# Kernel optimization log

Measured on AMD Instinct MI355X. Metric: run time of the kernel, lower is better.

The kernel has to match this reference:

```python
import jax, jax.numpy as jnp
import numpy as np
import math

B, S, H = 4, 2048, 1024
EMBED_DIM = 1024


def setup_inputs() -> dict:
    key = jax.random.key(0)
    ks = jax.random.split(key, 7)
    scale = 1.0 / math.sqrt(H)
    return {
        "xs": jax.random.normal(ks[0], (B, S, H), dtype=jnp.float32),
        "WQ_w": jax.random.normal(ks[1], (EMBED_DIM, H), dtype=jnp.float32) * scale,
        "WQ_b": jax.random.normal(ks[2], (EMBED_DIM,), dtype=jnp.float32) * scale,
        "WK_w": jax.random.normal(ks[3], (EMBED_DIM, H), dtype=jnp.float32) * scale,
        "WK_b": jax.random.normal(ks[4], (EMBED_DIM,), dtype=jnp.float32) * scale,
        "WV_w": jax.random.normal(ks[5], (EMBED_DIM, H), dtype=jnp.float32) * scale,
        "WV_b": jax.random.normal(ks[6], (EMBED_DIM,), dtype=jnp.float32) * scale,
    }


def reference(xs, WQ_w, WQ_b, WK_w, WK_b, WV_w, WV_b):
    # Linear projections (torch nn.Linear: x @ W.T + b)
    q = jnp.einsum('bsh,eh->bse', xs, WQ_w) + WQ_b  # [B,S,E]
    k = jnp.einsum('bsh,eh->bse', xs, WK_w) + WK_b
    v = jnp.einsum('bsh,eh->bse', xs, WV_w) + WV_b
    seq_len = xs.shape[1]
    inv_sqrt_e = 1.0 / math.sqrt(EMBED_DIM)
    qk = jnp.einsum('bqe,bke->bqk', q, k) * inv_sqrt_e  # [B,S,S]
    # causal mask: positions k > q get -inf (triu, diagonal=1)
    causal = jnp.tril(jnp.ones((seq_len, seq_len), dtype=bool))
    qk = jnp.where(causal[None, :, :], qk, -jnp.inf)
    attn = jax.nn.softmax(qk, axis=2)
    y = jnp.einsum('bqk,bke->bqe', attn, v)  # [B,S,E]
    return y
```

## Files before the change

kernel.cpp:

```cpp
#include <hip/hip_runtime.h>
#include <cstdint>
#include <cstddef>

typedef _Float16 f16;
typedef __attribute__((ext_vector_type(4))) _Float16 f16x4;
typedef __attribute__((ext_vector_type(8))) _Float16 f16x8;
typedef __attribute__((ext_vector_type(4))) float f32x4;

static constexpr int BB = 4;
static constexpr int SS = 2048;
static constexpr int EE = 1024;

static constexpr int BM = 128, BN = 128, BK = 32;

__device__ __forceinline__ void gload_lds16(const f16* g, f16* l) {
  __builtin_amdgcn_global_load_lds(
      (const __attribute__((address_space(1))) void*)g,
      (__attribute__((address_space(3))) void*)l, 16, 0, 0);
}

struct Frag {
  int lane, wave, wy, wx, l16, quad;
  __device__ Frag() {
    const int tid = threadIdx.x;
    lane = tid & 63; wave = tid >> 6;
    wy = wave >> 1; wx = wave & 1;
    l16 = lane & 15; quad = lane >> 4;
  }
};

__device__ __forceinline__ void gemm_core(
    const f16* __restrict__ A, const f16* __restrict__ Bt,
    int lda, int ldb, int kTiles,
    f16* __restrict__ Ash, f16* __restrict__ Bsh,
    f32x4 acc[4][4], const Frag& fr)
{
  const int ca0 = fr.wave * 128 + fr.lane;
  const int ca1 = ca0 + 64;
  const int ra0 = ca0 >> 2, ka0 = (ca0 & 3) << 3;
  const int ra1 = ca1 >> 2, ka1 = (ca1 & 3) << 3;

  const f16* gA0 = A + (size_t)ra0 * lda + ka0;
  const f16* gA1 = A + (size_t)ra1 * lda + ka1;
  const f16* gB0 = Bt + (size_t)ra0 * ldb + ka0;
  const f16* gB1 = Bt + (size_t)ra1 * ldb + ka1;
  f16* lA0 = Ash + ca0 * 8;
  f16* lA1 = Ash + ca1 * 8;
  f16* lB0 = Bsh + ca0 * 8;
  f16* lB1 = Bsh + ca1 * 8;

  for (int kt = 0; kt < kTiles; ++kt) {
    const int ko = kt * BK;
    gload_lds16(gA0 + ko, lA0);
    gload_lds16(gA1 + ko, lA1);
    gload_lds16(gB0 + ko, lB0);
    gload_lds16(gB1 + ko, lB1);
    __syncthreads();
    f16x8 af[4], bf[4];
#pragma unroll
    for (int mi = 0; mi < 4; ++mi)
      af[mi] = *(const f16x8*)(Ash + (fr.wy * 64 + mi * 16 + fr.l16) * BK + fr.quad * 8);
#pragma unroll
    for (int ni = 0; ni < 4; ++ni)
      bf[ni] = *(const f16x8*)(Bsh + (fr.wx * 64 + ni * 16 + fr.l16) * BK + fr.quad * 8);
#pragma unroll
    for (int mi = 0; mi < 4; ++mi)
#pragma unroll
      for (int ni = 0; ni < 4; ++ni)
        acc[mi][ni] = __builtin_amdgcn_mfma_f32_16x16x32_f16(af[mi], bf[ni], acc[mi][ni], 0, 0, 0);
    __syncthreads();
  }
}

__global__ __launch_bounds__(256) void cast_kernel(
    const float* __restrict__ in, f16* __restrict__ out, int n4)
{
  const int i = blockIdx.x * 256 + threadIdx.x;
  if (i < n4) {
    const float4 f = ((const float4*)in)[i];
    f16x4 h;
    h.x = (f16)f.x; h.y = (f16)f.y; h.z = (f16)f.z; h.w = (f16)f.w;
    ((f16x4*)out)[i] = h;
  }
}

__global__ __launch_bounds__(256) void cast_w_kernel(
    const float* __restrict__ w0, const float* __restrict__ w1, const float* __restrict__ w2,
    f16* __restrict__ o0, f16* __restrict__ o1, f16* __restrict__ o2, int n4)
{
  const int z = blockIdx.y;
  const float* in = (z == 0) ? w0 : (z == 1) ? w1 : w2;
  f16* out = (z == 0) ? o0 : (z == 1) ? o1 : o2;
  const int i = blockIdx.x * 256 + threadIdx.x;
  if (i < n4) {
    const float4 f = ((const float4*)in)[i];
    f16x4 h;
    h.x = (f16)f.x; h.y = (f16)f.y; h.z = (f16)f.z; h.w = (f16)f.w;
    ((f16x4*)out)[i] = h;
  }
}

__global__ __launch_bounds__(256, 4) void qkv_kernel(
    const f16* __restrict__ X,
    const f16* __restrict__ W0, const f16* __restrict__ W1, const f16* __restrict__ W2,
    const float* __restrict__ b0, const float* __restrict__ b1, const float* __restrict__ b2,
    f16* __restrict__ O0, f16* __restrict__ O1, f16* __restrict__ O2)
{
  __shared__ __align__(16) f16 Ash[BM * BK];
  __shared__ __align__(16) f16 Bsh[BN * BK];
  const int z = blockIdx.z;
  const f16* W = (z == 0) ? W0 : (z == 1) ? W1 : W2;
  const float* bias = (z == 0) ? b0 : (z == 1) ? b1 : b2;
  f16* out = (z == 0) ? O0 : (z == 1) ? O1 : O2;
  const int row0 = blockIdx.x * BM, col0 = blockIdx.y * BN;
  Frag fr;
  f32x4 acc[4][4] = {};
  gemm_core(X + (size_t)row0 * EE, W + (size_t)col0 * EE, EE, EE, EE / BK, Ash, Bsh, acc, fr);
#pragma unroll
  for (int ni = 0; ni < 4; ++ni) {
    const int c = col0 + fr.wx * 64 + ni * 16 + fr.l16;
    const float bv = bias[c];
#pragma unroll
    for (int mi = 0; mi < 4; ++mi) {
      const int r = row0 + fr.wy * 64 + mi * 16 + fr.quad * 4;
#pragma unroll
      for (int i = 0; i < 4; ++i)
        out[(size_t)(r + i) * EE + c] = (f16)(acc[mi][ni][i] + bv);
    }
  }
}

__global__ __launch_bounds__(256) void transpose_kernel(
    const f16* __restrict__ V, f16* __restrict__ Vt)
{
  __shared__ __align__(16) f16 t[64][68];
  const int b = blockIdx.z;
  const int s0 = blockIdx.x * 64, e0 = blockIdx.y * 64;
  const int tid = threadIdx.x;
  const int r = tid >> 4;
  const int c4 = (tid & 15) << 2;
  const f16* src = V + (size_t)b * SS * EE;
  f16* dst = Vt + (size_t)b * EE * SS;
#pragma unroll
  for (int i = 0; i < 4; ++i) {
    const int row = i * 16 + r;
    const f16x4 v = *(const f16x4*)(src + (size_t)(s0 + row) * EE + e0 + c4);
    *(f16x4*)&t[row][c4] = v;
  }
  __syncthreads();
#pragma unroll
  for (int i = 0; i < 4; ++i) {
    const int row = i * 16 + r;
    f16x4 v;
    v.x = t[c4 + 0][row]; v.y = t[c4 + 1][row];
    v.z = t[c4 + 2][row]; v.w = t[c4 + 3][row];
    *(f16x4*)(dst + (size_t)(e0 + row) * SS + s0 + c4) = v;
  }
}

__global__ __launch_bounds__(256, 4) void scores_kernel(
    const f16* __restrict__ Q, const f16* __restrict__ Kh, f16* __restrict__ Sc)
{
  __shared__ __align__(16) f16 Ash[BM * BK];
  __shared__ __align__(16) f16 Bsh[BN * BK];
  const int t = blockIdx.x, b = blockIdx.z;
  int qt = 0;
  while ((qt + 1) * (qt + 2) / 2 <= t) ++qt;
  const int kt = t - qt * (qt + 1) / 2;
  const f16* A  = Q  + (size_t)b * SS * EE + (size_t)qt * BM * EE;
  const f16* Bp = Kh + (size_t)b * SS * EE + (size_t)kt * BN * EE;
  f16* out = Sc + (size_t)b * SS * SS;
  Frag fr;
  f32x4 acc[4][4] = {};
  gemm_core(A, Bp, EE, EE, EE / BK, Ash, Bsh, acc, fr);
  const float scale = 0.03125f;
#pragma unroll
  for (int ni = 0; ni < 4; ++ni) {
    const int c = kt * BN + fr.wx * 64 + ni * 16 + fr.l16;
#pragma unroll
    for (int mi = 0; mi < 4; ++mi) {
      const int r = qt * BM + fr.wy * 64 + mi * 16 + fr.quad * 4;
#pragma unroll
      for (int i = 0; i < 4; ++i)
        out[(size_t)(r + i) * SS + c] = (f16)(acc[mi][ni][i] * scale);
    }
  }
}

__global__ __launch_bounds__(256) void softmax_kernel(f16* __restrict__ Sc)
{
  const int q = blockIdx.x, b = blockIdx.y;
  f16* row = Sc + (size_t)b * SS * SS + (size_t)q * SS;
  const int n = q + 1;
  const int kend = ((q >> 7) + 1) << 7;
  const int tid = threadIdx.x;
  const int i0 = tid * 8;

  float v[8];
  if (i0 + 8 <= n) {
    const f16x8 h = *(const f16x8*)(row + i0);
#pragma unroll
    for (int j = 0; j < 8; ++j) v[j] = (float)h[j];
  } else {
#pragma unroll
    for (int j = 0; j < 8; ++j) {
      const int idx = i0 + j;
      v[j] = (idx < n) ? (float)row[idx] : -1e30f;
    }
  }

  float m = v[0];
#pragma unroll
  for (int j = 1; j < 8; ++j) m = fmaxf(m, v[j]);
  __shared__ float red[4];
#pragma unroll
  for (int off = 32; off > 0; off >>= 1) m = fmaxf(m, __shfl_down(m, off));
  if ((tid & 63) == 0) red[tid >> 6] = m;
  __syncthreads();
  m = fmaxf(fmaxf(red[0], red[1]), fmaxf(red[2], red[3]));

  float sum = 0.f;
#pragma unroll
  for (int j = 0; j < 8; ++j) {
    v[j] = (i0 + j < n) ? __expf(v[j] - m) : 0.f;
    sum += v[j];
  }
#pragma unroll
  for (int off = 32; off > 0; off >>= 1) sum += __shfl_down(sum, off);
  __syncthreads();
  if ((tid & 63) == 0) red[tid >> 6] = sum;
  __syncthreads();
  sum = red[0] + red[1] + red[2] + red[3];
  const float inv = 1.f / sum;

  if (i0 < kend) {
    f16x8 h;
#pragma unroll
    for (int j = 0; j < 8; ++j) h[j] = (f16)(v[j] * inv);
    *(f16x8*)(row + i0) = h;
  }
}

__global__ __launch_bounds__(256, 4) void pv_kernel(
    const f16* __restrict__ P, const f16* __restrict__ Vt, float* __restrict__ Y)
{
  __shared__ __align__(16) f16 Ash[BM * BK];
  __shared__ __align__(16) f16 Bsh[BN * BK];
  const int qt = (gridDim.x - 1) - blockIdx.x, et = blockIdx.y, b = blockIdx.z;
  const f16* A  = P  + (size_t)b * SS * SS + (size_t)qt * BM * SS;
  const f16* Bp = Vt + (size_t)b * EE * SS + (size_t)et * BN * SS;
  float* out = Y + (size_t)b * SS * EE;
  Frag fr;
  f32x4 acc[4][4] = {};
  gemm_core(A, Bp, SS, SS, (qt + 1) * (BM / BK), Ash, Bsh, acc, fr);
#pragma unroll
  for (int ni = 0; ni < 4; ++ni) {
    const int c = et * BN + fr.wx * 64 + ni * 16 + fr.l16;
#pragma unroll
    for (int mi = 0; mi < 4; ++mi) {
      const int r = qt * BM + fr.wy * 64 + mi * 16 + fr.quad * 4;
#pragma unroll
      for (int i = 0; i < 4; ++i)
        out[(size_t)(r + i) * EE + c] = acc[mi][ni][i];
    }
  }
}

extern "C" void kernel_launch(void* const* d_in, const int* in_sizes, int n_in,
                              void* d_out, int out_size, void* d_ws, size_t ws_size,
                              hipStream_t stream)
{
  const float* xs  = (const float*)d_in[0];
  const float* WQw = (const float*)d_in[1];
  const float* WQb = (const float*)d_in[2];
  const float* WKw = (const float*)d_in[3];
  const float* WKb = (const float*)d_in[4];
  const float* WVw = (const float*)d_in[5];
  const float* WVb = (const float*)d_in[6];

  const size_t ME = (size_t)BB * SS * EE;
  const size_t WE = (size_t)EE * EE;

  f16* Xh = (f16*)d_ws;
  f16* Wq = Xh + ME;
  f16* Wk = Wq + WE;
  f16* Wv = Wk + WE;
  f16* Qh = Wv + WE;
  f16* Kh = Qh + ME;
  f16* Vh = Kh + ME;
  f16* Vt = Vh + ME;
  f16* Sc = Vt + ME;

  cast_kernel<<<dim3((unsigned)(ME / 4 / 256)), 256, 0, stream>>>(xs, Xh, (int)(ME / 4));
  cast_w_kernel<<<dim3((unsigned)(WE / 4 / 256), 3), 256, 0, stream>>>(
      WQw, WKw, WVw, Wq, Wk, Wv, (int)(WE / 4));

  qkv_kernel<<<dim3((BB * SS) / BM, EE / BN, 3), 256, 0, stream>>>(
      Xh, Wq, Wk, Wv, WQb, WKb, WVb, Qh, Kh, Vh);
  transpose_kernel<<<dim3(SS / 64, EE / 64, BB), 256, 0, stream>>>(Vh, Vt);
  const int nTri = (SS / BM) * (SS / BM + 1) / 2;
  scores_kernel<<<dim3(nTri, 1, BB), 256, 0, stream>>>(Qh, Kh, Sc);
  softmax_kernel<<<dim3(SS, BB), 256, 0, stream>>>(Sc);
  pv_kernel<<<dim3(SS / BM, EE / BN, BB), 256, 0, stream>>>(Sc, Vt, (float*)d_out);
}
```

Baseline: 267.8 us.

## Switch GEMMs to 256x128 tiles with 32x32x16 MFMA and swizzled LDS

Enlarges the shared GEMM core's block tile to 256x128 and moves from 16x16x32 to 32x32x16 MFMA, so each wave computes a 128x64 sub-tile from fewer LDS fragment loads. It adds an XOR swizzle on the K-chunk index of the LDS layout to cut bank conflicts. The causal score tiling, softmax padding and PV loop bounds are adjusted to the 256-row query tiles. The cost is more accumulator registers (occupancy hint drops from 4 to 2 blocks), coarser causal granularity that computes more masked-out work, and fewer blocks in the grids.

```diff
diff --git a/kernel.cpp b/kernel.cpp
--- a/kernel.cpp
+++ b/kernel.cpp
@@ -5,13 +5,13 @@
 typedef _Float16 f16;
 typedef __attribute__((ext_vector_type(4))) _Float16 f16x4;
 typedef __attribute__((ext_vector_type(8))) _Float16 f16x8;
-typedef __attribute__((ext_vector_type(4))) float f32x4;
+typedef __attribute__((ext_vector_type(16))) float f32x16;
 
 static constexpr int BB = 4;
 static constexpr int SS = 2048;
 static constexpr int EE = 1024;
 
-static constexpr int BM = 128, BN = 128, BK = 32;
+static constexpr int BM = 256, BN = 128, BK = 32;
 
 __device__ __forceinline__ void gload_lds16(const f16* g, f16* l) {
   __builtin_amdgcn_global_load_lds(
@@ -20,54 +20,69 @@
 }
 
 struct Frag {
-  int lane, wave, wy, wx, l16, quad;
+  int lane, wave, wy, wx, l32, lh;
   __device__ Frag() {
     const int tid = threadIdx.x;
     lane = tid & 63; wave = tid >> 6;
     wy = wave >> 1; wx = wave & 1;
-    l16 = lane & 15; quad = lane >> 4;
+    l32 = lane & 31; lh = lane >> 5;
   }
 };
 
 __device__ __forceinline__ void gemm_core(
     const f16* __restrict__ A, const f16* __restrict__ Bt,
-    int lda, int ldb, int kTiles,
+    int lda, int ldb, int kIters,
     f16* __restrict__ Ash, f16* __restrict__ Bsh,
-    f32x4 acc[4][4], const Frag& fr)
-{
-  const int ca0 = fr.wave * 128 + fr.lane;
-  const int ca1 = ca0 + 64;
-  const int ra0 = ca0 >> 2, ka0 = (ca0 & 3) << 3;
-  const int ra1 = ca1 >> 2, ka1 = (ca1 & 3) << 3;
-
-  const f16* gA0 = A + (size_t)ra0 * lda + ka0;
-  const f16* gA1 = A + (size_t)ra1 * lda + ka1;
-  const f16* gB0 = Bt + (size_t)ra0 * ldb + ka0;
-  const f16* gB1 = Bt + (size_t)ra1 * ldb + ka1;
-  f16* lA0 = Ash + ca0 * 8;
-  f16* lA1 = Ash + ca1 * 8;
-  f16* lB0 = Bsh + ca0 * 8;
-  f16* lB1 = Bsh + ca1 * 8;
-
-  for (int kt = 0; kt < kTiles; ++kt) {
+    f32x16 acc[4][2], const Frag& fr)
+{
+  const f16* gA[4]; f16* lA[4];
+#pragma unroll
+  for (int i = 0; i < 4; ++i) {
+    const int c = fr.wave * 256 + i * 64 + fr.lane;
+    const int row = c >> 2;
+    const int kc = (c & 3) ^ (row & 3);
+    gA[i] = A + (size_t)row * lda + kc * 8;
+    lA[i] = Ash + c * 8;
+  }
+  const f16* gB[2]; f16* lB[2];
+#pragma unroll
+  for (int i = 0; i < 2; ++i) {
+    const int c = fr.wave * 128 + i * 64 + fr.lane;
+    const int row = c >> 2;
+    const int kc = (c & 3) ^ (row & 3);
+    gB[i] = Bt + (size_t)row * ldb + kc * 8;
+    lB[i] = Bsh + c * 8;
+  }
+  int aoff[2], boff[2];
+#pragma unroll
+  for (int ks = 0; ks < 2; ++ks) {
+    const int perm = ((ks * 2 + fr.lh) ^ (fr.l32 & 3)) * 8;
+    aoff[ks] = (fr.wy * 128 + fr.l32) * 32 + perm;
+    boff[ks] = (fr.wx * 64 + fr.l32) * 32 + perm;
+  }
+
+  for (int kt = 0; kt < kIters; ++kt) {
     const int ko = kt * BK;
-    gload_lds16(gA0 + ko, lA0);
-    gload_lds16(gA1 + ko, lA1);
-    gload_lds16(gB0 + ko, lB0);
-    gload_lds16(gB1 + ko, lB1);
+#pragma unroll
+    for (int i = 0; i < 4; ++i) gload_lds16(gA[i] + ko, lA[i]);
+#pragma unroll
+    for (int i = 0; i < 2; ++i) gload_lds16(gB[i] + ko, lB[i]);
     __syncthreads();
-    f16x8 af[4], bf[4];
-#pragma unroll
-    for (int mi = 0; mi < 4; ++mi)
-      af[mi] = *(const f16x8*)(Ash + (fr.wy * 64 + mi * 16 + fr.l16) * BK + fr.quad * 8);
-#pragma unroll
-    for (int ni = 0; ni < 4; ++ni)
-      bf[ni] = *(const f16x8*)(Bsh + (fr.wx * 64 + ni * 16 + fr.l16) * BK + fr.quad * 8);
-#pragma unroll
-    for (int mi = 0; mi < 4; ++mi)
-#pragma unroll
-      for (int ni = 0; ni < 4; ++ni)
-        acc[mi][ni] = __builtin_amdgcn_mfma_f32_16x16x32_f16(af[mi], bf[ni], acc[mi][ni], 0, 0, 0);
+#pragma unroll
+    for (int ks = 0; ks < 2; ++ks) {
+      f16x8 af[4], bf[2];
+#pragma unroll
+      for (int mi = 0; mi < 4; ++mi)
+        af[mi] = *(const f16x8*)(Ash + aoff[ks] + mi * 32 * 32);
+#pragma unroll
+      for (int ni = 0; ni < 2; ++ni)
+        bf[ni] = *(const f16x8*)(Bsh + boff[ks] + ni * 32 * 32);
+#pragma unroll
+      for (int mi = 0; mi < 4; ++mi)
+#pragma unroll
+        for (int ni = 0; ni < 2; ++ni)
+          acc[mi][ni] = __builtin_amdgcn_mfma_f32_32x32x16_f16(af[mi], bf[ni], acc[mi][ni], 0, 0, 0);
+    }
     __syncthreads();
   }
 }
@@ -100,7 +115,7 @@
   }
 }
 
-__global__ __launch_bounds__(256, 4) void qkv_kernel(
+__global__ __launch_bounds__(256, 2) void qkv_kernel(
     const f16* __restrict__ X,
     const f16* __restrict__ W0, const f16* __restrict__ W1, const f16* __restrict__ W2,
     const float* __restrict__ b0, const float* __restrict__ b1, const float* __restrict__ b2,
@@ -114,18 +129,20 @@
   f16* out = (z == 0) ? O0 : (z == 1) ? O1 : O2;
   const int row0 = blockIdx.x * BM, col0 = blockIdx.y * BN;
   Frag fr;
-  f32x4 acc[4][4] = {};
+  f32x16 acc[4][2] = {};
   gemm_core(X + (size_t)row0 * EE, W + (size_t)col0 * EE, EE, EE, EE / BK, Ash, Bsh, acc, fr);
 #pragma unroll
-  for (int ni = 0; ni < 4; ++ni) {
-    const int c = col0 + fr.wx * 64 + ni * 16 + fr.l16;
+  for (int ni = 0; ni < 2; ++ni) {
+    const int c = col0 + fr.wx * 64 + ni * 32 + fr.l32;
     const float bv = bias[c];
 #pragma unroll
     for (int mi = 0; mi < 4; ++mi) {
-      const int r = row0 + fr.wy * 64 + mi * 16 + fr.quad * 4;
-#pragma unroll
-      for (int i = 0; i < 4; ++i)
-        out[(size_t)(r + i) * EE + c] = (f16)(acc[mi][ni][i] + bv);
+      const int rbase = row0 + fr.wy * 128 + mi * 32 + fr.lh * 4;
+#pragma unroll
+      for (int i = 0; i < 16; ++i) {
+        const int r = rbase + (i & 3) + 8 * (i >> 2);
+        out[(size_t)r * EE + c] = (f16)(acc[mi][ni][i] + bv);
+      }
     }
   }
 }
@@ -158,31 +175,33 @@
   }
 }
 
-__global__ __launch_bounds__(256, 4) void scores_kernel(
+__global__ __launch_bounds__(256, 2) void scores_kernel(
     const f16* __restrict__ Q, const f16* __restrict__ Kh, f16* __restrict__ Sc)
 {
   __shared__ __align__(16) f16 Ash[BM * BK];
   __shared__ __align__(16) f16 Bsh[BN * BK];
   const int t = blockIdx.x, b = blockIdx.z;
   int qt = 0;
-  while ((qt + 1) * (qt + 2) / 2 <= t) ++qt;
-  const int kt = t - qt * (qt + 1) / 2;
+  while ((qt + 1) * (qt + 2) <= t) ++qt;
+  const int kt = t - qt * (qt + 1);
   const f16* A  = Q  + (size_t)b * SS * EE + (size_t)qt * BM * EE;
   const f16* Bp = Kh + (size_t)b * SS * EE + (size_t)kt * BN * EE;
   f16* out = Sc + (size_t)b * SS * SS;
   Frag fr;
-  f32x4 acc[4][4] = {};
+  f32x16 acc[4][2] = {};
   gemm_core(A, Bp, EE, EE, EE / BK, Ash, Bsh, acc, fr);
   const float scale = 0.03125f;
 #pragma unroll
-  for (int ni = 0; ni < 4; ++ni) {
-    const int c = kt * BN + fr.wx * 64 + ni * 16 + fr.l16;
+  for (int ni = 0; ni < 2; ++ni) {
+    const int c = kt * BN + fr.wx * 64 + ni * 32 + fr.l32;
 #pragma unroll
     for (int mi = 0; mi < 4; ++mi) {
-      const int r = qt * BM + fr.wy * 64 + mi * 16 + fr.quad * 4;
-#pragma unroll
-      for (int i = 0; i < 4; ++i)
-        out[(size_t)(r + i) * SS + c] = (f16)(acc[mi][ni][i] * scale);
+      const int rbase = qt * BM + fr.wy * 128 + mi * 32 + fr.lh * 4;
+#pragma unroll
+      for (int i = 0; i < 16; ++i) {
+        const int r = rbase + (i & 3) + 8 * (i >> 2);
+        out[(size_t)r * SS + c] = (f16)(acc[mi][ni][i] * scale);
+      }
     }
   }
 }
@@ -192,7 +211,7 @@
   const int q = blockIdx.x, b = blockIdx.y;
   f16* row = Sc + (size_t)b * SS * SS + (size_t)q * SS;
   const int n = q + 1;
-  const int kend = ((q >> 7) + 1) << 7;
+  const int kend = ((q >> 8) + 1) << 8;
   const int tid = threadIdx.x;
   const int i0 = tid * 8;
 
@@ -241,7 +260,7 @@
   }
 }
 
-__global__ __launch_bounds__(256, 4) void pv_kernel(
+__global__ __launch_bounds__(256, 2) void pv_kernel(
     const f16* __restrict__ P, const f16* __restrict__ Vt, float* __restrict__ Y)
 {
   __shared__ __align__(16) f16 Ash[BM * BK];
@@ -251,17 +270,19 @@
   const f16* Bp = Vt + (size_t)b * EE * SS + (size_t)et * BN * SS;
   float* out = Y + (size_t)b * SS * EE;
   Frag fr;
-  f32x4 acc[4][4] = {};
+  f32x16 acc[4][2] = {};
   gemm_core(A, Bp, SS, SS, (qt + 1) * (BM / BK), Ash, Bsh, acc, fr);
 #pragma unroll
-  for (int ni = 0; ni < 4; ++ni) {
-    const int c = et * BN + fr.wx * 64 + ni * 16 + fr.l16;
+  for (int ni = 0; ni < 2; ++ni) {
+    const int c = et * BN + fr.wx * 64 + ni * 32 + fr.l32;
 #pragma unroll
     for (int mi = 0; mi < 4; ++mi) {
-      const int r = qt * BM + fr.wy * 64 + mi * 16 + fr.quad * 4;
-#pragma unroll
-      for (int i = 0; i < 4; ++i)
-        out[(size_t)(r + i) * EE + c] = acc[mi][ni][i];
+      const int rbase = qt * BM + fr.wy * 128 + mi * 32 + fr.lh * 4;
+#pragma unroll
+      for (int i = 0; i < 16; ++i) {
+        const int r = rbase + (i & 3) + 8 * (i >> 2);
+        out[(size_t)r * EE + c] = acc[mi][ni][i];
+      }
     }
   }
 }
@@ -298,7 +319,8 @@
   qkv_kernel<<<dim3((BB * SS) / BM, EE / BN, 3), 256, 0, stream>>>(
       Xh, Wq, Wk, Wv, WQb, WKb, WVb, Qh, Kh, Vh);
   transpose_kernel<<<dim3(SS / 64, EE / 64, BB), 256, 0, stream>>>(Vh, Vt);
-  const int nTri = (SS / BM) * (SS / BM + 1) / 2;
+  const int nQT = SS / BM;
+  const int nTri = nQT * (nQT + 1);
   scores_kernel<<<dim3(nTri, 1, BB), 256, 0, stream>>>(Qh, Kh, Sc);
   softmax_kernel<<<dim3(SS, BB), 256, 0, stream>>>(Sc);
   pv_kernel<<<dim3(SS / BM, EE / BN, BB), 256, 0, stream>>>(Sc, Vt, (float*)d_out);
```

Result: slower. 309.2 us (+15.4%).

## Fuse Q/K/V projections into one kernel sharing the X tile

Applied to the files above, without the earlier changes.

Replaces the three-way z-grid QKV GEMM with a single kernel that loads each X tile into LDS once and multiplies it against all three weight tiles, keeping three accumulator sets. This cuts redundant X global loads and LDS fills by a factor of three. In exchange it triples accumulator registers, lowering the occupancy target to 2, and launches a third as many blocks. It also drops the min-blocks occupancy hint from the scores and pv kernels.

```diff
diff --git a/kernel.cpp b/kernel.cpp
--- a/kernel.cpp
+++ b/kernel.cpp
@@ -100,32 +100,80 @@
   }
 }
 
-__global__ __launch_bounds__(256, 4) void qkv_kernel(
+__global__ __launch_bounds__(256, 2) void qkv_fused_kernel(
     const f16* __restrict__ X,
     const f16* __restrict__ W0, const f16* __restrict__ W1, const f16* __restrict__ W2,
     const float* __restrict__ b0, const float* __restrict__ b1, const float* __restrict__ b2,
     f16* __restrict__ O0, f16* __restrict__ O1, f16* __restrict__ O2)
 {
   __shared__ __align__(16) f16 Ash[BM * BK];
-  __shared__ __align__(16) f16 Bsh[BN * BK];
-  const int z = blockIdx.z;
-  const f16* W = (z == 0) ? W0 : (z == 1) ? W1 : W2;
-  const float* bias = (z == 0) ? b0 : (z == 1) ? b1 : b2;
-  f16* out = (z == 0) ? O0 : (z == 1) ? O1 : O2;
+  __shared__ __align__(16) f16 Bsh[3][BN * BK];
   const int row0 = blockIdx.x * BM, col0 = blockIdx.y * BN;
   Frag fr;
-  f32x4 acc[4][4] = {};
-  gemm_core(X + (size_t)row0 * EE, W + (size_t)col0 * EE, EE, EE, EE / BK, Ash, Bsh, acc, fr);
-#pragma unroll
-  for (int ni = 0; ni < 4; ++ni) {
-    const int c = col0 + fr.wx * 64 + ni * 16 + fr.l16;
-    const float bv = bias[c];
-#pragma unroll
-    for (int mi = 0; mi < 4; ++mi) {
-      const int r = row0 + fr.wy * 64 + mi * 16 + fr.quad * 4;
-#pragma unroll
-      for (int i = 0; i < 4; ++i)
-        out[(size_t)(r + i) * EE + c] = (f16)(acc[mi][ni][i] + bv);
+
+  const int ca0 = fr.wave * 128 + fr.lane;
+  const int ca1 = ca0 + 64;
+  const int ra0 = ca0 >> 2, ka0 = (ca0 & 3) << 3;
+  const int ra1 = ca1 >> 2, ka1 = (ca1 & 3) << 3;
+
+  const f16* gA0 = X + (size_t)(row0 + ra0) * EE + ka0;
+  const f16* gA1 = X + (size_t)(row0 + ra1) * EE + ka1;
+  const f16* gW[3][2];
+  gW[0][0] = W0 + (size_t)(col0 + ra0) * EE + ka0;
+  gW[0][1] = W0 + (size_t)(col0 + ra1) * EE + ka1;
+  gW[1][0] = W1 + (size_t)(col0 + ra0) * EE + ka0;
+  gW[1][1] = W1 + (size_t)(col0 + ra1) * EE + ka1;
+  gW[2][0] = W2 + (size_t)(col0 + ra0) * EE + ka0;
+  gW[2][1] = W2 + (size_t)(col0 + ra1) * EE + ka1;
+  f16* lA0 = Ash + ca0 * 8;
+  f16* lA1 = Ash + ca1 * 8;
+
+  f32x4 acc[3][4][4] = {};
+
+  for (int kt = 0; kt < EE / BK; ++kt) {
+    const int ko = kt * BK;
+    gload_lds16(gA0 + ko, lA0);
+    gload_lds16(gA1 + ko, lA1);
+#pragma unroll
+    for (int z = 0; z < 3; ++z) {
+      gload_lds16(gW[z][0] + ko, Bsh[z] + ca0 * 8);
+      gload_lds16(gW[z][1] + ko, Bsh[z] + ca1 * 8);
+    }
+    __syncthreads();
+    f16x8 af[4];
+#pragma unroll
+    for (int mi = 0; mi < 4; ++mi)
+      af[mi] = *(const f16x8*)(Ash + (fr.wy * 64 + mi * 16 + fr.l16) * BK + fr.quad * 8);
+#pragma unroll
+    for (int z = 0; z < 3; ++z) {
+      f16x8 bf[4];
+#pragma unroll
+      for (int ni = 0; ni < 4; ++ni)
+        bf[ni] = *(const f16x8*)(Bsh[z] + (fr.wx * 64 + ni * 16 + fr.l16) * BK + fr.quad * 8);
+#pragma unroll
+      for (int mi = 0; mi < 4; ++mi)
+#pragma unroll
+        for (int ni = 0; ni < 4; ++ni)
+          acc[z][mi][ni] = __builtin_amdgcn_mfma_f32_16x16x32_f16(af[mi], bf[ni], acc[z][mi][ni], 0, 0, 0);
+    }
+    __syncthreads();
+  }
+
+#pragma unroll
+  for (int z = 0; z < 3; ++z) {
+    const float* bias = (z == 0) ? b0 : (z == 1) ? b1 : b2;
+    f16* out = (z == 0) ? O0 : (z == 1) ? O1 : O2;
+#pragma unroll
+    for (int ni = 0; ni < 4; ++ni) {
+      const int c = col0 + fr.wx * 64 + ni * 16 + fr.l16;
+      const float bv = bias[c];
+#pragma unroll
+      for (int mi = 0; mi < 4; ++mi) {
+        const int r = row0 + fr.wy * 64 + mi * 16 + fr.quad * 4;
+#pragma unroll
+        for (int i = 0; i < 4; ++i)
+          out[(size_t)(r + i) * EE + c] = (f16)(acc[z][mi][ni][i] + bv);
+      }
     }
   }
 }
@@ -158,7 +206,7 @@
   }
 }
 
-__global__ __launch_bounds__(256, 4) void scores_kernel(
+__global__ __launch_bounds__(256) void scores_kernel(
     const f16* __restrict__ Q, const f16* __restrict__ Kh, f16* __restrict__ Sc)
 {
   __shared__ __align__(16) f16 Ash[BM * BK];
@@ -241,7 +289,7 @@
   }
 }
 
-__global__ __launch_bounds__(256, 4) void pv_kernel(
+__global__ __launch_bounds__(256) void pv_kernel(
     const f16* __restrict__ P, const f16* __restrict__ Vt, float* __restrict__ Y)
 {
   __shared__ __align__(16) f16 Ash[BM * BK];
@@ -295,7 +343,7 @@
   cast_w_kernel<<<dim3((unsigned)(WE / 4 / 256), 3), 256, 0, stream>>>(
       WQw, WKw, WVw, Wq, Wk, Wv, (int)(WE / 4));
 
-  qkv_kernel<<<dim3((BB * SS) / BM, EE / BN, 3), 256, 0, stream>>>(
+  qkv_fused_kernel<<<dim3((BB * SS) / BM, EE / BN), 256, 0, stream>>>(
       Xh, Wq, Wk, Wv, WQb, WKb, WVb, Qh, Kh, Vh);
   transpose_kernel<<<dim3(SS / 64, EE / 64, BB), 256, 0, stream>>>(Vh, Vt);
   const int nTri = (SS / BM) * (SS / BM + 1) / 2;
```

New measurement: 265.3 us. No clear change (-0.9%).
